# Optimization experiments

Hardware: AMD Instinct MI355X
Metric: run time of the kernel (lower is better)

Reference implementation:

```python
import jax, jax.numpy as jnp
import numpy as np

ALPHA = 0.1        # self.alpha in the torch module
NUM_CLASSES = 10   # predict_acc hardcodes range(10)


def _sqdist(x, centers):
    # Faithful to sum((x - c)**2, -1) but computed via the gemm identity to
    # avoid materializing the (N, K, D) broadcast the torch code creates.
    x2 = jnp.sum(x * x, axis=1, keepdims=True)          # [N, 1]
    c2 = jnp.sum(centers * centers, axis=1)             # [K]
    d = x2 + c2[None, :] - 2.0 * (x @ centers.T)        # [N, K]
    return jnp.maximum(d, 0.0)                          # clamp fp round-off


def _predict_acc(distance, y):
    n = distance.shape[0]
    y_p = jnp.argmin(distance, axis=1)                  # index[1][:, 0]
    # counts[i, c] = #points assigned to cluster i (only i < 10 matter) with label c
    onehot_cluster = (y_p[:, None] == jnp.arange(NUM_CLASSES)[None, :]).astype(jnp.float32)  # [N, 10]
    onehot_label = (y[:, None] == jnp.arange(NUM_CLASSES)[None, :]).astype(jnp.float32)      # [N, 10]
    counts = onehot_cluster.T @ onehot_label            # [10, 10]
    used = jnp.zeros((NUM_CLASSES,), dtype=bool)
    correct = jnp.float32(0.0)
    for i in range(NUM_CLASSES):
        bin_i = counts[i]
        has_points = jnp.sum(bin_i) > 0                 # empty bincount -> 'continue'
        label = jnp.argmax(bin_i)                       # first max index, like where(bin==max)[0][0]
        # quchong: recursively zero already-used labels == argmax with used masked out
        masked = jnp.where(used, 0.0, bin_i)
        label = jnp.where(used[label], jnp.argmax(masked), label)
        correct = correct + jnp.where(has_points, bin_i[label], 0.0)
        used = jnp.where(has_points, used.at[label].set(True), used)
    return correct / jnp.float32(n)


def setup_inputs() -> dict:
    key = jax.random.key(0)
    kx, ky, kc = jax.random.split(key, 3)
    N, K, D = 262144, 256, 64
    x = jax.random.normal(kx, (N, D), dtype=jnp.float32)
    y = jax.random.randint(ky, (N,), 0, 10, dtype=jnp.int64)
    centers = jax.random.normal(kc, (K, D), dtype=jnp.float32)
    return {"x": x, "y": y, "centers": centers}


def reference(x, y, centers):
    distance = _sqdist(x, centers)                      # caldis, op='l2'
    # calwei: exp(-alpha*log(d+1)) then row-normalize
    we = jnp.exp(-ALPHA * jnp.log1p(distance))
    weight = we / jnp.sum(we, axis=1, keepdims=True)
    loss = jnp.sum(weight * distance)                   # calloss
    acc = _predict_acc(distance, y)
    return (loss, acc)
```

## Files before the change

### kernel.cpp

```cpp
#include <hip/hip_runtime.h>

#define ALPHA 0.1f
#define NUM_CLASSES 10

typedef __attribute__((ext_vector_type(8))) short bf16x8;
typedef __attribute__((ext_vector_type(4))) float f32x4;


__device__ __forceinline__ unsigned pack2(float a, float b) {
    return (__float_as_uint(b) & 0xFFFF0000u) | (__float_as_uint(a) >> 16);
}
__device__ __forceinline__ float truncbf(float a) {
    return __uint_as_float(__float_as_uint(a) & 0xFFFF0000u);
}

__global__ __launch_bounds__(512, 4) void dist_kernel(
    const float* __restrict__ x,
    const int*   __restrict__ y,
    const float* __restrict__ centers,
    float* __restrict__ loss_acc,
    unsigned int* __restrict__ counts,
    int NT)
{
    __shared__ __align__(16) char bstage[4 * 4 * 64 * 16];
    __shared__ float x2s[128];
    __shared__ float c2s[256];
    __shared__ float    comb_swe[8][128];
    __shared__ float    comb_swd[8][128];
    __shared__ unsigned comb_best[8][128];
    __shared__ unsigned counts_l[100];

    const int tid  = threadIdx.x;
    const int w    = tid >> 6;
    const int lane = tid & 63;
    const int q    = lane >> 4;
    const int r    = lane & 15;

    if (tid < 100) counts_l[tid] = 0u;

    if (tid < 256) {
        const float4* crow = (const float4*)(centers + tid * 64);
        float s = 0.f;
#pragma unroll
        for (int j = 0; j < 16; ++j) {
            float4 v = crow[j];
            s = fmaf(v.x, v.x, s); s = fmaf(v.y, v.y, s);
            s = fmaf(v.z, v.z, s); s = fmaf(v.w, v.w, s);
        }
        c2s[tid] = s;
    }

    bf16x8 af[2][4];
#pragma unroll
    for (int ct = 0; ct < 2; ++ct) {
        const int row = w * 32 + ct * 16 + r;
        const float4* C = (const float4*)(centers + (size_t)row * 64);
        float4 v0 = C[q * 2], v1 = C[q * 2 + 1];
        float4 v2 = C[8 + q * 2], v3 = C[9 + q * 2];
        float4 m0 = make_float4(-2.f * v0.x, -2.f * v0.y, -2.f * v0.z, -2.f * v0.w);
        float4 m1 = make_float4(-2.f * v1.x, -2.f * v1.y, -2.f * v1.z, -2.f * v1.w);
        float4 m2 = make_float4(-2.f * v2.x, -2.f * v2.y, -2.f * v2.z, -2.f * v2.w);
        float4 m3 = make_float4(-2.f * v3.x, -2.f * v3.y, -2.f * v3.z, -2.f * v3.w);
        union { bf16x8 v; unsigned u[4]; } h0, h1, l0, l1;
        h0.u[0] = pack2(m0.x, m0.y); h0.u[1] = pack2(m0.z, m0.w);
        h0.u[2] = pack2(m1.x, m1.y); h0.u[3] = pack2(m1.z, m1.w);
        h1.u[0] = pack2(m2.x, m2.y); h1.u[1] = pack2(m2.z, m2.w);
        h1.u[2] = pack2(m3.x, m3.y); h1.u[3] = pack2(m3.z, m3.w);
        l0.u[0] = pack2(m0.x - truncbf(m0.x), m0.y - truncbf(m0.y));
        l0.u[1] = pack2(m0.z - truncbf(m0.z), m0.w - truncbf(m0.w));
        l0.u[2] = pack2(m1.x - truncbf(m1.x), m1.y - truncbf(m1.y));
        l0.u[3] = pack2(m1.z - truncbf(m1.z), m1.w - truncbf(m1.w));
        l1.u[0] = pack2(m2.x - truncbf(m2.x), m2.y - truncbf(m2.y));
        l1.u[1] = pack2(m2.z - truncbf(m2.z), m2.w - truncbf(m2.w));
        l1.u[2] = pack2(m3.x - truncbf(m3.x), m3.y - truncbf(m3.y));
        l1.u[3] = pack2(m3.z - truncbf(m3.z), m3.w - truncbf(m3.w));
        af[ct][0] = h0.v; af[ct][1] = h1.v; af[ct][2] = l0.v; af[ct][3] = l1.v;
    }

    float4 pv0, pv1, pv2, pv3;
    {
        const int row = blockIdx.x * 128 + w * 16 + r;
        const float4* X = (const float4*)(x + (size_t)row * 64);
        pv0 = X[q * 2]; pv1 = X[q * 2 + 1];
        pv2 = X[8 + q * 2]; pv3 = X[9 + q * 2];
    }

    __syncthreads();

    float c2r1[2][4];
#pragma unroll
    for (int ct = 0; ct < 2; ++ct) {
        float4 v = *(const float4*)(c2s + w * 32 + ct * 16 + q * 4);
        c2r1[ct][0] = v.x + 1.f; c2r1[ct][1] = v.y + 1.f;
        c2r1[ct][2] = v.z + 1.f; c2r1[ct][3] = v.w + 1.f;
    }

    float loss_local = 0.f;

    for (int t = blockIdx.x; t < NT; t += gridDim.x) {
        int ylab = 0;
        if (tid < 128) ylab = y[t * 128 + tid];
        const int tn = t + gridDim.x;

        if (w < 4) {
            float4 v0 = pv0, v1 = pv1, v2 = pv2, v3 = pv3;
            if (tn < NT) {
                const int row = tn * 128 + w * 16 + r;
                const float4* X = (const float4*)(x + (size_t)row * 64);
                pv0 = X[q * 2]; pv1 = X[q * 2 + 1];
                pv2 = X[8 + q * 2]; pv3 = X[9 + q * 2];
            }

            float p = v0.x * v0.x;
            p = fmaf(v0.y, v0.y, p); p = fmaf(v0.z, v0.z, p); p = fmaf(v0.w, v0.w, p);
            p = fmaf(v1.x, v1.x, p); p = fmaf(v1.y, v1.y, p); p = fmaf(v1.z, v1.z, p); p = fmaf(v1.w, v1.w, p);
            p = fmaf(v2.x, v2.x, p); p = fmaf(v2.y, v2.y, p); p = fmaf(v2.z, v2.z, p); p = fmaf(v2.w, v2.w, p);
            p = fmaf(v3.x, v3.x, p); p = fmaf(v3.y, v3.y, p); p = fmaf(v3.z, v3.z, p); p = fmaf(v3.w, v3.w, p);
            p += __shfl_xor(p, 16);
            p += __shfl_xor(p, 32);
            if (q == 0) x2s[w * 16 + r] = p;

            union { bf16x8 v; uint4 u4; unsigned u[4]; } h0, h1, l0, l1;
            h0.u[0] = pack2(v0.x, v0.y); h0.u[1] = pack2(v0.z, v0.w);
            h0.u[2] = pack2(v1.x, v1.y); h0.u[3] = pack2(v1.z, v1.w);
            h1.u[0] = pack2(v2.x, v2.y); h1.u[1] = pack2(v2.z, v2.w);
            h1.u[2] = pack2(v3.x, v3.y); h1.u[3] = pack2(v3.z, v3.w);
            l0.u[0] = pack2(v0.x - truncbf(v0.x), v0.y - truncbf(v0.y));
            l0.u[1] = pack2(v0.z - truncbf(v0.z), v0.w - truncbf(v0.w));
            l0.u[2] = pack2(v1.x - truncbf(v1.x), v1.y - truncbf(v1.y));
            l0.u[3] = pack2(v1.z - truncbf(v1.z), v1.w - truncbf(v1.w));
            l1.u[0] = pack2(v2.x - truncbf(v2.x), v2.y - truncbf(v2.y));
            l1.u[1] = pack2(v2.z - truncbf(v2.z), v2.w - truncbf(v2.w));
            l1.u[2] = pack2(v3.x - truncbf(v3.x), v3.y - truncbf(v3.y));
            l1.u[3] = pack2(v3.z - truncbf(v3.z), v3.w - truncbf(v3.w));
            *(uint4*)(bstage + (((w * 4 + 0) * 64 + lane) << 4)) = h0.u4;
            *(uint4*)(bstage + (((w * 4 + 1) * 64 + lane) << 4)) = h1.u4;
            *(uint4*)(bstage + (((w * 4 + 2) * 64 + lane) << 4)) = l0.u4;
            *(uint4*)(bstage + (((w * 4 + 3) * 64 + lane) << 4)) = l1.u4;
        }
        __syncthreads();

#pragma unroll
        for (int pt = 0; pt < 4; ++pt) {
            union { uint4 u4; bf16x8 v; } b0, b1, b2, b3;
            b0.u4 = *(const uint4*)(bstage + (((pt * 4 + 0) * 64 + lane) << 4));
            b1.u4 = *(const uint4*)(bstage + (((pt * 4 + 1) * 64 + lane) << 4));
            b2.u4 = *(const uint4*)(bstage + (((pt * 4 + 2) * 64 + lane) << 4));
            b3.u4 = *(const uint4*)(bstage + (((pt * 4 + 3) * 64 + lane) << 4));
            const float x2p = x2s[pt * 16 + r];

            f32x4 acc[2];
#pragma unroll
            for (int ct = 0; ct < 2; ++ct) {
                f32x4 a;
                a[0] = x2p + c2r1[ct][0]; a[1] = x2p + c2r1[ct][1];
                a[2] = x2p + c2r1[ct][2]; a[3] = x2p + c2r1[ct][3];
                a = __builtin_amdgcn_mfma_f32_16x16x32_bf16(af[ct][0], b0.v, a, 0, 0, 0);
                a = __builtin_amdgcn_mfma_f32_16x16x32_bf16(af[ct][1], b1.v, a, 0, 0, 0);
                a = __builtin_amdgcn_mfma_f32_16x16x32_bf16(af[ct][2], b0.v, a, 0, 0, 0);
                a = __builtin_amdgcn_mfma_f32_16x16x32_bf16(af[ct][3], b1.v, a, 0, 0, 0);
                a = __builtin_amdgcn_mfma_f32_16x16x32_bf16(af[ct][0], b2.v, a, 0, 0, 0);
                a = __builtin_amdgcn_mfma_f32_16x16x32_bf16(af[ct][1], b3.v, a, 0, 0, 0);
                acc[ct] = a;
            }

            float swe = 0.f, swdu = 0.f;
            unsigned best = 0xFFFFFFFFu;
#pragma unroll
            for (int ct = 0; ct < 2; ++ct) {
#pragma unroll
                for (int reg = 0; reg < 4; ++reg) {
                    const float u = acc[ct][reg];
                    const unsigned kid = (unsigned)(w * 32 + ct * 16 + q * 4 + reg);
                    best = min(best, (__float_as_uint(u) & 0xFFFFFF00u) | kid);
                    float wg = exp2f(-ALPHA * __log2f(u));
                    swe += wg;
                    swdu = fmaf(wg, u, swdu);
                }
            }
            swe += __shfl_xor(swe, 16); swe += __shfl_xor(swe, 32);
            swdu += __shfl_xor(swdu, 16); swdu += __shfl_xor(swdu, 32);
            best = min(best, (unsigned)__shfl_xor((int)best, 16));
            best = min(best, (unsigned)__shfl_xor((int)best, 32));
            if (q == 0) {
                comb_swe[w][pt * 16 + r]  = swe;
                comb_swd[w][pt * 16 + r]  = swdu;
                comb_best[w][pt * 16 + r] = best;
            }
        }
        __syncthreads();

        if (w >= 4) {
            float4 v0 = pv0, v1 = pv1, v2 = pv2, v3 = pv3;
            if (tn < NT) {
                const int row = tn * 128 + w * 16 + r;
                const float4* X = (const float4*)(x + (size_t)row * 64);
                pv0 = X[q * 2]; pv1 = X[q * 2 + 1];
                pv2 = X[8 + q * 2]; pv3 = X[9 + q * 2];
            }

            float p = v0.x * v0.x;
            p = fmaf(v0.y, v0.y, p); p = fmaf(v0.z, v0.z, p); p = fmaf(v0.w, v0.w, p);
            p = fmaf(v1.x, v1.x, p); p = fmaf(v1.y, v1.y, p); p = fmaf(v1.z, v1.z, p); p = fmaf(v1.w, v1.w, p);
            p = fmaf(v2.x, v2.x, p); p = fmaf(v2.y, v2.y, p); p = fmaf(v2.z, v2.z, p); p = fmaf(v2.w, v2.w, p);
            p = fmaf(v3.x, v3.x, p); p = fmaf(v3.y, v3.y, p); p = fmaf(v3.z, v3.z, p); p = fmaf(v3.w, v3.w, p);
            p += __shfl_xor(p, 16);
            p += __shfl_xor(p, 32);
            if (q == 0) x2s[w * 16 + r] = p;

            union { bf16x8 v; uint4 u4; unsigned u[4]; } h0, h1, l0, l1;
            h0.u[0] = pack2(v0.x, v0.y); h0.u[1] = pack2(v0.z, v0.w);
            h0.u[2] = pack2(v1.x, v1.y); h0.u[3] = pack2(v1.z, v1.w);
            h1.u[0] = pack2(v2.x, v2.y); h1.u[1] = pack2(v2.z, v2.w);
            h1.u[2] = pack2(v3.x, v3.y); h1.u[3] = pack2(v3.z, v3.w);
            l0.u[0] = pack2(v0.x - truncbf(v0.x), v0.y - truncbf(v0.y));
            l0.u[1] = pack2(v0.z - truncbf(v0.z), v0.w - truncbf(v0.w));
            l0.u[2] = pack2(v1.x - truncbf(v1.x), v1.y - truncbf(v1.y));
            l0.u[3] = pack2(v1.z - truncbf(v1.z), v1.w - truncbf(v1.w));
            l1.u[0] = pack2(v2.x - truncbf(v2.x), v2.y - truncbf(v2.y));
            l1.u[1] = pack2(v2.z - truncbf(v2.z), v2.w - truncbf(v2.w));
            l1.u[2] = pack2(v3.x - truncbf(v3.x), v3.y - truncbf(v3.y));
            l1.u[3] = pack2(v3.z - truncbf(v3.z), v3.w - truncbf(v3.w));
            *(uint4*)(bstage + ((((w - 4) * 4 + 0) * 64 + lane) << 4)) = h0.u4;
            *(uint4*)(bstage + ((((w - 4) * 4 + 1) * 64 + lane) << 4)) = h1.u4;
            *(uint4*)(bstage + ((((w - 4) * 4 + 2) * 64 + lane) << 4)) = l0.u4;
            *(uint4*)(bstage + ((((w - 4) * 4 + 3) * 64 + lane) << 4)) = l1.u4;
        }
        __syncthreads();

#pragma unroll
        for (int pt = 0; pt < 4; ++pt) {
            union { uint4 u4; bf16x8 v; } b0, b1, b2, b3;
            b0.u4 = *(const uint4*)(bstage + (((pt * 4 + 0) * 64 + lane) << 4));
            b1.u4 = *(const uint4*)(bstage + (((pt * 4 + 1) * 64 + lane) << 4));
            b2.u4 = *(const uint4*)(bstage + (((pt * 4 + 2) * 64 + lane) << 4));
            b3.u4 = *(const uint4*)(bstage + (((pt * 4 + 3) * 64 + lane) << 4));
            const float x2p = x2s[64 + pt * 16 + r];

            f32x4 acc[2];
#pragma unroll
            for (int ct = 0; ct < 2; ++ct) {
                f32x4 a;
                a[0] = x2p + c2r1[ct][0]; a[1] = x2p + c2r1[ct][1];
                a[2] = x2p + c2r1[ct][2]; a[3] = x2p + c2r1[ct][3];
                a = __builtin_amdgcn_mfma_f32_16x16x32_bf16(af[ct][0], b0.v, a, 0, 0, 0);
                a = __builtin_amdgcn_mfma_f32_16x16x32_bf16(af[ct][1], b1.v, a, 0, 0, 0);
                a = __builtin_amdgcn_mfma_f32_16x16x32_bf16(af[ct][2], b0.v, a, 0, 0, 0);
                a = __builtin_amdgcn_mfma_f32_16x16x32_bf16(af[ct][3], b1.v, a, 0, 0, 0);
                a = __builtin_amdgcn_mfma_f32_16x16x32_bf16(af[ct][0], b2.v, a, 0, 0, 0);
                a = __builtin_amdgcn_mfma_f32_16x16x32_bf16(af[ct][1], b3.v, a, 0, 0, 0);
                acc[ct] = a;
            }

            float swe = 0.f, swdu = 0.f;
            unsigned best = 0xFFFFFFFFu;
#pragma unroll
            for (int ct = 0; ct < 2; ++ct) {
#pragma unroll
                for (int reg = 0; reg < 4; ++reg) {
                    const float u = acc[ct][reg];
                    const unsigned kid = (unsigned)(w * 32 + ct * 16 + q * 4 + reg);
                    best = min(best, (__float_as_uint(u) & 0xFFFFFF00u) | kid);
                    float wg = exp2f(-ALPHA * __log2f(u));
                    swe += wg;
                    swdu = fmaf(wg, u, swdu);
                }
            }
            swe += __shfl_xor(swe, 16); swe += __shfl_xor(swe, 32);
            swdu += __shfl_xor(swdu, 16); swdu += __shfl_xor(swdu, 32);
            best = min(best, (unsigned)__shfl_xor((int)best, 16));
            best = min(best, (unsigned)__shfl_xor((int)best, 32));
            if (q == 0) {
                comb_swe[w][64 + pt * 16 + r]  = swe;
                comb_swd[w][64 + pt * 16 + r]  = swdu;
                comb_best[w][64 + pt * 16 + r] = best;
            }
        }
        __syncthreads();

        if (tid < 128) {
            float SWE = comb_swe[0][tid], SWD = comb_swd[0][tid];
            unsigned BEST = comb_best[0][tid];
#pragma unroll
            for (int g = 1; g < 8; ++g) {
                SWE += comb_swe[g][tid];
                SWD += comb_swd[g][tid];
                BEST = min(BEST, comb_best[g][tid]);
            }
            loss_local += SWD / SWE - 1.f;
            const unsigned bk = BEST & 0xFFu;
            if (bk < NUM_CLASSES) {
                atomicAdd(&counts_l[bk * NUM_CLASSES + ylab], 1u);
            }
        }
    }

    if (w < 2) {
        float v = loss_local;
#pragma unroll
        for (int o = 32; o > 0; o >>= 1) v += __shfl_down(v, o);
        if (lane == 0) atomicAdd(loss_acc, v);
    }

    __syncthreads();
    if (tid < 100) {
        const unsigned c = counts_l[tid];
        if (c) atomicAdd(&counts[tid], c);
    }
}


__global__ void finalize_kernel(
    const float* __restrict__ loss_acc,
    const unsigned int* __restrict__ counts,
    float* __restrict__ out,
    int N)
{
    __shared__ float cs[NUM_CLASSES * NUM_CLASSES];
    __shared__ float ls;
    const int tid = threadIdx.x;
    if (tid < NUM_CLASSES * NUM_CLASSES) cs[tid] = (float)counts[tid];
    if (tid == NUM_CLASSES * NUM_CLASSES) ls = loss_acc[0];
    __syncthreads();
    if (tid == 0) {
        bool used[NUM_CLASSES];
        for (int i = 0; i < NUM_CLASSES; ++i) used[i] = false;

        float correct = 0.f;
        for (int i = 0; i < NUM_CLASSES; ++i) {
            const float* ci = cs + i * NUM_CLASSES;
            float rowsum = 0.f;
            for (int j = 0; j < NUM_CLASSES; ++j) rowsum += ci[j];
            bool has_points = rowsum > 0.f;

            int label = 0;
            float mx = ci[0];
            for (int j = 1; j < NUM_CLASSES; ++j)
                if (ci[j] > mx) { mx = ci[j]; label = j; }

            if (used[label]) {
                float mm = used[0] ? 0.f : ci[0];
                int l2 = 0;
                for (int j = 1; j < NUM_CLASSES; ++j) {
                    float v = used[j] ? 0.f : ci[j];
                    if (v > mm) { mm = v; l2 = j; }
                }
                label = l2;
            }

            if (has_points) {
                correct += ci[label];
                used[label] = true;
            }
        }
        out[0] = ls;
        out[1] = correct / (float)N;
    }
}


extern "C" void kernel_launch(void* const* d_in, const int* in_sizes, int n_in,
                              void* d_out, int out_size, void* d_ws, size_t ws_size,
                              hipStream_t stream)
{
    const float* x       = (const float*)d_in[0];
    const int*   y       = (const int*)d_in[1];
    const float* centers = (const float*)d_in[2];
    float* out = (float*)d_out;

    const int N  = in_sizes[0] / 64;
    const int NT = N / 128;

    float* loss          = (float*)d_ws;
    unsigned int* counts = (unsigned int*)((char*)d_ws + 4);

    hipMemsetAsync(d_ws, 0, 512, stream);

    int grid = 1024;
    if (grid > NT) grid = NT;
    dist_kernel<<<grid, 512, 0, stream>>>(x, y, centers, loss, counts, NT);

    finalize_kernel<<<1, 128, 0, stream>>>(loss, counts, out, N);
}
```

Measured before the change: 150.5 us.

## Defer per-tile reduction into next iteration and fuse finalize via last-block ticket

The per-row combine of partial sums and argmin for tile t moves into iteration t+1, where warps 6-7 (which previously idled during x staging) run it alongside the staging by warps 0-3. This removes one serialized phase between barriers. The separate finalize kernel is dropped: the last block to take an atomic ticket reads the global counts and loss and computes the outputs, saving a kernel launch. The risks are extra threadfence and atomic traffic and reliance on correct memory ordering between blocks.

```diff
diff --git a/kernel.cpp b/kernel.cpp
--- a/kernel.cpp
+++ b/kernel.cpp
@@ -20,7 +20,9 @@
     const float* __restrict__ centers,
     float* __restrict__ loss_acc,
     unsigned int* __restrict__ counts,
-    int NT)
+    unsigned int* __restrict__ ticket,
+    float* __restrict__ out,
+    int NT, int NPTS)
 {
     __shared__ __align__(16) char bstage[4 * 4 * 64 * 16];
     __shared__ float x2s[128];
@@ -29,6 +31,9 @@
     __shared__ float    comb_swd[8][128];
     __shared__ unsigned comb_best[8][128];
     __shared__ unsigned counts_l[100];
+    __shared__ float    fin_cs[100];
+    __shared__ float    fin_ls;
+    __shared__ unsigned fin_flag;
 
     const int tid  = threadIdx.x;
     const int w    = tid >> 6;
@@ -96,10 +101,12 @@
     }
 
     float loss_local = 0.f;
+    int ylab_prev = 0;
+    bool have_prev = false;
 
     for (int t = blockIdx.x; t < NT; t += gridDim.x) {
         int ylab = 0;
-        if (tid < 128) ylab = y[t * 128 + tid];
+        if (tid >= 384) ylab = y[t * 128 + (tid - 384)];
         const int tn = t + gridDim.x;
 
         if (w < 4) {
@@ -138,6 +145,23 @@
             *(uint4*)(bstage + (((w * 4 + 2) * 64 + lane) << 4)) = l0.u4;
             *(uint4*)(bstage + (((w * 4 + 3) * 64 + lane) << 4)) = l1.u4;
         }
+
+        if (have_prev && tid >= 384) {
+            const int p = tid - 384;
+            float SWE = comb_swe[0][p], SWD = comb_swd[0][p];
+            unsigned BEST = comb_best[0][p];
+#pragma unroll
+            for (int g = 1; g < 8; ++g) {
+                SWE += comb_swe[g][p];
+                SWD += comb_swd[g][p];
+                BEST = min(BEST, comb_best[g][p]);
+            }
+            loss_local += SWD / SWE - 1.f;
+            const unsigned bk = BEST & 0xFFu;
+            if (bk < NUM_CLASSES) {
+                atomicAdd(&counts_l[bk * NUM_CLASSES + ylab_prev], 1u);
+            }
+        }
         __syncthreads();
 
 #pragma unroll
@@ -278,24 +302,28 @@
         }
         __syncthreads();
 
-        if (tid < 128) {
-            float SWE = comb_swe[0][tid], SWD = comb_swd[0][tid];
-            unsigned BEST = comb_best[0][tid];
-#pragma unroll
-            for (int g = 1; g < 8; ++g) {
-                SWE += comb_swe[g][tid];
-                SWD += comb_swd[g][tid];
-                BEST = min(BEST, comb_best[g][tid]);
-            }
-            loss_local += SWD / SWE - 1.f;
-            const unsigned bk = BEST & 0xFFu;
-            if (bk < NUM_CLASSES) {
-                atomicAdd(&counts_l[bk * NUM_CLASSES + ylab], 1u);
-            }
-        }
-    }
-
-    if (w < 2) {
+        ylab_prev = ylab;
+        have_prev = true;
+    }
+
+    if (have_prev && tid >= 384) {
+        const int p = tid - 384;
+        float SWE = comb_swe[0][p], SWD = comb_swd[0][p];
+        unsigned BEST = comb_best[0][p];
+#pragma unroll
+        for (int g = 1; g < 8; ++g) {
+            SWE += comb_swe[g][p];
+            SWD += comb_swd[g][p];
+            BEST = min(BEST, comb_best[g][p]);
+        }
+        loss_local += SWD / SWE - 1.f;
+        const unsigned bk = BEST & 0xFFu;
+        if (bk < NUM_CLASSES) {
+            atomicAdd(&counts_l[bk * NUM_CLASSES + ylab_prev], 1u);
+        }
+    }
+
+    if (w >= 6) {
         float v = loss_local;
 #pragma unroll
         for (int o = 32; o > 0; o >>= 1) v += __shfl_down(v, o);
@@ -307,54 +335,50 @@
         const unsigned c = counts_l[tid];
         if (c) atomicAdd(&counts[tid], c);
     }
-}
-
-
-__global__ void finalize_kernel(
-    const float* __restrict__ loss_acc,
-    const unsigned int* __restrict__ counts,
-    float* __restrict__ out,
-    int N)
-{
-    __shared__ float cs[NUM_CLASSES * NUM_CLASSES];
-    __shared__ float ls;
-    const int tid = threadIdx.x;
-    if (tid < NUM_CLASSES * NUM_CLASSES) cs[tid] = (float)counts[tid];
-    if (tid == NUM_CLASSES * NUM_CLASSES) ls = loss_acc[0];
+    __threadfence();
     __syncthreads();
+
     if (tid == 0) {
-        bool used[NUM_CLASSES];
-        for (int i = 0; i < NUM_CLASSES; ++i) used[i] = false;
-
-        float correct = 0.f;
-        for (int i = 0; i < NUM_CLASSES; ++i) {
-            const float* ci = cs + i * NUM_CLASSES;
-            float rowsum = 0.f;
-            for (int j = 0; j < NUM_CLASSES; ++j) rowsum += ci[j];
-            bool has_points = rowsum > 0.f;
-
-            int label = 0;
-            float mx = ci[0];
-            for (int j = 1; j < NUM_CLASSES; ++j)
-                if (ci[j] > mx) { mx = ci[j]; label = j; }
-
-            if (used[label]) {
-                float mm = used[0] ? 0.f : ci[0];
-                int l2 = 0;
-                for (int j = 1; j < NUM_CLASSES; ++j) {
-                    float v = used[j] ? 0.f : ci[j];
-                    if (v > mm) { mm = v; l2 = j; }
+        fin_flag = (atomicAdd(ticket, 1u) == (unsigned)(gridDim.x - 1)) ? 1u : 0u;
+    }
+    __syncthreads();
+    if (fin_flag) {
+        if (tid < 100) fin_cs[tid] = (float)atomicAdd(&counts[tid], 0u);
+        if (tid == 100) fin_ls = atomicAdd(loss_acc, 0.f);
+        __syncthreads();
+        if (tid == 0) {
+            bool used[NUM_CLASSES];
+            for (int i = 0; i < NUM_CLASSES; ++i) used[i] = false;
+            float correct = 0.f;
+            for (int i = 0; i < NUM_CLASSES; ++i) {
+                const float* ci = fin_cs + i * NUM_CLASSES;
+                float rowsum = 0.f;
+                for (int j = 0; j < NUM_CLASSES; ++j) rowsum += ci[j];
+                bool has_points = rowsum > 0.f;
+
+                int label = 0;
+                float mx = ci[0];
+                for (int j = 1; j < NUM_CLASSES; ++j)
+                    if (ci[j] > mx) { mx = ci[j]; label = j; }
+
+                if (used[label]) {
+                    float mm = used[0] ? 0.f : ci[0];
+                    int l2 = 0;
+                    for (int j = 1; j < NUM_CLASSES; ++j) {
+                        float v = used[j] ? 0.f : ci[j];
+                        if (v > mm) { mm = v; l2 = j; }
+                    }
+                    label = l2;
                 }
-                label = l2;
-            }
-
-            if (has_points) {
-                correct += ci[label];
-                used[label] = true;
-            }
-        }
-        out[0] = ls;
-        out[1] = correct / (float)N;
+
+                if (has_points) {
+                    correct += ci[label];
+                    used[label] = true;
+                }
+            }
+            out[0] = fin_ls;
+            out[1] = correct / (float)NPTS;
+        }
     }
 }
 
@@ -373,12 +397,12 @@
 
     float* loss          = (float*)d_ws;
     unsigned int* counts = (unsigned int*)((char*)d_ws + 4);
+    unsigned int* ticket = (unsigned int*)((char*)d_ws + 448);
 
     hipMemsetAsync(d_ws, 0, 512, stream);
 
     int grid = 1024;
     if (grid > NT) grid = NT;
-    dist_kernel<<<grid, 512, 0, stream>>>(x, y, centers, loss, counts, NT);
-
-    finalize_kernel<<<1, 128, 0, stream>>>(loss, counts, out, N);
+    dist_kernel<<<grid, 512, 0, stream>>>(x, y, centers, loss, counts, ticket,
+                                          out, NT, N);
 }
```

Result: slower. 248.9 us (+65.4%).
